# Kernel optimization log

Measured on AMD Instinct MI355X. Metric: run time of the kernel, lower is better.

## Reference

```python
import jax, jax.numpy as jnp
import numpy as np

B, S, D, H = 2, 2048, 2048, 16
HD = D // H
SCALE = 1.0 / np.sqrt(HD)


def setup_inputs() -> dict:
    key = jax.random.key(0)
    ks = jax.random.split(key, 11)
    xav = np.sqrt(6.0 / (D + D))  # xavier uniform bound for square weights
    def w(k):
        return jax.random.uniform(k, (D, D), jnp.float32, -xav, xav)
    return {
        "query": jax.random.normal(ks[0], (B, S, D), jnp.float32),
        "key": jax.random.normal(ks[1], (B, S, D), jnp.float32),
        "value": jax.random.normal(ks[2], (B, S, D), jnp.float32),
        "Wq": w(ks[3]), "bq": jnp.zeros((D,), jnp.float32),
        "Wk": w(ks[4]), "bk": jnp.zeros((D,), jnp.float32),
        "Wv": w(ks[5]), "bv": jnp.zeros((D,), jnp.float32),
        "Wo": w(ks[6]), "bo": jnp.zeros((D,), jnp.float32),
    }


def reference(query, key, value, Wq, bq, Wk, bk, Wv, bv, Wo, bo):
    # projections (torch Linear: x @ W.T + b)
    q = query @ Wq.T + bq
    k = key @ Wk.T + bk
    v = value @ Wv.T + bv
    # [B, H, S, HD]
    q = q.reshape(B, S, H, HD).transpose(0, 2, 1, 3)
    k = k.reshape(B, S, H, HD).transpose(0, 2, 1, 3)
    v = v.reshape(B, S, H, HD).transpose(0, 2, 1, 3)
    scores = jnp.einsum("bhqd,bhkd->bhqk", q, k) * SCALE
    causal = jnp.triu(jnp.ones((S, S), bool), k=1)
    scores = jnp.where(causal, -jnp.inf, scores)
    attn = jax.nn.softmax(scores, axis=-1)  # dropout p=0.0 -> identity
    out = jnp.einsum("bhqk,bhkd->bhqd", attn, v)
    out = out.transpose(0, 2, 1, 3).reshape(B, S, D)
    return out @ Wo.T + bo
```

## Files before the change

### kernel.cpp

```cpp
#include <hip/hip_runtime.h>
#include <hip/hip_bf16.h>


#define LOG2E 1.44269504088896340736f

typedef __attribute__((ext_vector_type(8))) short short8;
typedef __attribute__((ext_vector_type(4))) short short4b;
typedef __attribute__((ext_vector_type(4))) float floatx4;

__device__ __forceinline__ short f2bf(float f) {
  unsigned int u = __builtin_bit_cast(unsigned int, f);
  u += 0x7FFFu + ((u >> 16) & 1u);
  return (short)(u >> 16);
}

__device__ __forceinline__ short4b pack4bf(float a, float b, float c, float d) {
  __hip_bfloat162 lo = __float22bfloat162_rn(float2{a, b});
  __hip_bfloat162 hi = __float22bfloat162_rn(float2{c, d});
  short4b r;
  r[0] = __builtin_bit_cast(short, lo.x); r[1] = __builtin_bit_cast(short, lo.y);
  r[2] = __builtin_bit_cast(short, hi.x); r[3] = __builtin_bit_cast(short, hi.y);
  return r;
}

__device__ __forceinline__ void gl_lds16(const void* g, void* l) {
  __builtin_amdgcn_global_load_lds(
      (const __attribute__((address_space(1))) unsigned int*)g,
      (__attribute__((address_space(3))) unsigned int*)l, 16, 0, 0);
}

__global__ __launch_bounds__(256) void cvt_k(
    const float* __restrict__ s0, const float* __restrict__ s1,
    const float* __restrict__ s2, const float* __restrict__ s3,
    unsigned short* __restrict__ d0, unsigned short* __restrict__ d1,
    unsigned short* __restrict__ d2, unsigned short* __restrict__ d3, int n)
{
  const float* s; unsigned short* d;
  switch (blockIdx.y) {
    case 0: s = s0; d = d0; break;
    case 1: s = s1; d = d1; break;
    case 2: s = s2; d = d2; break;
    default: s = s3; d = d3; break;
  }
  const int i = (blockIdx.x * 256 + threadIdx.x) * 8;
  if (i >= n) return;
  float4 a = *(const float4*)(s + i);
  float4 b = *(const float4*)(s + i + 4);
  short8 v = (short8){f2bf(a.x), f2bf(a.y), f2bf(a.z), f2bf(a.w),
                      f2bf(b.x), f2bf(b.y), f2bf(b.z), f2bf(b.w)};
  *(short8*)(d + i) = v;
}

template<bool OUT_BF16, bool VT_OUT>
__global__ __launch_bounds__(512, 1) void gemm8_k(
    const unsigned short* __restrict__ A, const unsigned short* __restrict__ Bt,
    const float* __restrict__ bias, void* __restrict__ Cptr,
    int M, int N, int K, float alpha)
{
  __shared__ __align__(16) unsigned short As[3][256 * 64];
  __shared__ __align__(16) unsigned short Bs[3][128 * 64];
  (void)M;

  const int tid  = threadIdx.x;
  const int lane = tid & 63;
  const int wave = tid >> 6;
  const int quad = lane >> 4;
  const int l16  = lane & 15;
  const int lx7  = l16 & 7;
  const int wm   = wave >> 1, wn = wave & 1;
  const long bm  = (long)blockIdx.y * 256;
  const long bn  = (long)blockIdx.x * 128;

  const unsigned short* gA[4]; int lAo[4];
  const unsigned short* gB[2]; int lBo[2];
#pragma unroll
  for (int j = 0; j < 4; ++j) {
    const int pa = ((j >> 1) * 16 + wave * 2 + (j & 1)) * 64 + lane;
    const int r = pa >> 3, cp = pa & 7, cs = cp ^ (r & 7);
    gA[j]  = A + (bm + r) * (long)K + cs * 8;
    lAo[j] = pa * 8;
  }
#pragma unroll
  for (int j = 0; j < 2; ++j) {
    const int pb = (wave * 2 + j) * 64 + lane;
    const int r = pb >> 3, cp = pb & 7, cs = cp ^ (r & 7);
    gB[j]  = Bt + (bn + r) * (long)K + cs * 8;
    lBo[j] = pb * 8;
  }

  floatx4 acc[4][4];
#pragma unroll
  for (int i = 0; i < 4; ++i)
#pragma unroll
    for (int j = 0; j < 4; ++j) acc[i][j] = (floatx4){0.f, 0.f, 0.f, 0.f};

  const int NT = K >> 6;

#pragma unroll
  for (int j = 0; j < 4; ++j) gl_lds16(gA[j], &As[0][lAo[j]]);
#pragma unroll
  for (int j = 0; j < 2; ++j) gl_lds16(gB[j], &Bs[0][lBo[j]]);
  if (NT > 1) {
#pragma unroll
    for (int j = 0; j < 4; ++j) gl_lds16(gA[j] + 64, &As[1][lAo[j]]);
#pragma unroll
    for (int j = 0; j < 2; ++j) gl_lds16(gB[j] + 64, &Bs[1][lBo[j]]);
    asm volatile("s_waitcnt vmcnt(6)" ::: "memory");
  } else {
    asm volatile("s_waitcnt vmcnt(0)" ::: "memory");
  }
  __builtin_amdgcn_s_barrier();

  int cur = 0;
  for (int t = 0; t < NT; ++t) {
    int nx2 = cur + 2; if (nx2 >= 3) nx2 -= 3;
    const long kk2 = (long)(t + 2) * 64;
    const bool st  = (t + 2) < NT;
    const unsigned short* Ab = As[cur];
    const unsigned short* Bb = Bs[cur];

    short8 af[4][2];
#pragma unroll
    for (int mt = 0; mt < 4; ++mt)
#pragma unroll
      for (int ks = 0; ks < 2; ++ks)
        af[mt][ks] = *(const short8*)&Ab[(wm * 64 + mt * 16 + l16) * 64 +
                                         (((ks * 4 + quad) ^ lx7) * 8)];
    short8 bf0, bf1;

    bf0 = *(const short8*)&Bb[(wn * 64 + l16) * 64 + (((quad) ^ lx7) * 8)];
    bf1 = *(const short8*)&Bb[(wn * 64 + l16) * 64 + (((4 + quad) ^ lx7) * 8)];
    if (st) { gl_lds16(gA[0] + kk2, &As[nx2][lAo[0]]);
              gl_lds16(gA[1] + kk2, &As[nx2][lAo[1]]); }
    __builtin_amdgcn_s_barrier();
    asm volatile("s_waitcnt lgkmcnt(0)");
    __builtin_amdgcn_s_setprio(1);
#pragma unroll
    for (int mt = 0; mt < 4; ++mt) {
      acc[mt][0] = __builtin_amdgcn_mfma_f32_16x16x32_bf16(af[mt][0], bf0, acc[mt][0], 0, 0, 0);
      acc[mt][0] = __builtin_amdgcn_mfma_f32_16x16x32_bf16(af[mt][1], bf1, acc[mt][0], 0, 0, 0);
    }
    __builtin_amdgcn_s_setprio(0);
    __builtin_amdgcn_s_barrier();

    bf0 = *(const short8*)&Bb[(wn * 64 + 16 + l16) * 64 + (((quad) ^ lx7) * 8)];
    bf1 = *(const short8*)&Bb[(wn * 64 + 16 + l16) * 64 + (((4 + quad) ^ lx7) * 8)];
    if (st) { gl_lds16(gA[2] + kk2, &As[nx2][lAo[2]]);
              gl_lds16(gA[3] + kk2, &As[nx2][lAo[3]]); }
    __builtin_amdgcn_s_barrier();
    asm volatile("s_waitcnt lgkmcnt(0)");
    __builtin_amdgcn_s_setprio(1);
#pragma unroll
    for (int mt = 0; mt < 4; ++mt) {
      acc[mt][1] = __builtin_amdgcn_mfma_f32_16x16x32_bf16(af[mt][0], bf0, acc[mt][1], 0, 0, 0);
      acc[mt][1] = __builtin_amdgcn_mfma_f32_16x16x32_bf16(af[mt][1], bf1, acc[mt][1], 0, 0, 0);
    }
    __builtin_amdgcn_s_setprio(0);
    __builtin_amdgcn_s_barrier();

    bf0 = *(const short8*)&Bb[(wn * 64 + 32 + l16) * 64 + (((quad) ^ lx7) * 8)];
    bf1 = *(const short8*)&Bb[(wn * 64 + 32 + l16) * 64 + (((4 + quad) ^ lx7) * 8)];
    if (st) { gl_lds16(gB[0] + kk2, &Bs[nx2][lBo[0]]);
              gl_lds16(gB[1] + kk2, &Bs[nx2][lBo[1]]); }
    __builtin_amdgcn_s_barrier();
    asm volatile("s_waitcnt lgkmcnt(0)");
    __builtin_amdgcn_s_setprio(1);
#pragma unroll
    for (int mt = 0; mt < 4; ++mt) {
      acc[mt][2] = __builtin_amdgcn_mfma_f32_16x16x32_bf16(af[mt][0], bf0, acc[mt][2], 0, 0, 0);
      acc[mt][2] = __builtin_amdgcn_mfma_f32_16x16x32_bf16(af[mt][1], bf1, acc[mt][2], 0, 0, 0);
    }
    __builtin_amdgcn_s_setprio(0);
    __builtin_amdgcn_s_barrier();

    bf0 = *(const short8*)&Bb[(wn * 64 + 48 + l16) * 64 + (((quad) ^ lx7) * 8)];
    bf1 = *(const short8*)&Bb[(wn * 64 + 48 + l16) * 64 + (((4 + quad) ^ lx7) * 8)];
    __builtin_amdgcn_s_barrier();
    asm volatile("s_waitcnt lgkmcnt(0)");
    __builtin_amdgcn_s_setprio(1);
#pragma unroll
    for (int mt = 0; mt < 4; ++mt) {
      acc[mt][3] = __builtin_amdgcn_mfma_f32_16x16x32_bf16(af[mt][0], bf0, acc[mt][3], 0, 0, 0);
      acc[mt][3] = __builtin_amdgcn_mfma_f32_16x16x32_bf16(af[mt][1], bf1, acc[mt][3], 0, 0, 0);
    }
    __builtin_amdgcn_s_setprio(0);
    if (t + 1 < NT) {
      if (st) asm volatile("s_waitcnt vmcnt(6)" ::: "memory");
      else    asm volatile("s_waitcnt vmcnt(0)" ::: "memory");
    }
    __builtin_amdgcn_s_barrier();

    cur = cur + 1 >= 3 ? 0 : cur + 1;
  }

  if (VT_OUT) {
    __syncthreads();
    unsigned short* Ct = &As[0][0];
#pragma unroll
    for (int nt = 0; nt < 4; ++nt) {
      const int col_l = wn * 64 + nt * 16 + l16;
      const float bval = bias[bn + col_l];
#pragma unroll
      for (int mt = 0; mt < 4; ++mt) {
        const int row_l = wm * 64 + mt * 16 + quad * 4;
#pragma unroll
        for (int rg = 0; rg < 4; ++rg)
          Ct[col_l * 264 + row_l + rg] = (unsigned short)f2bf((acc[mt][nt][rg] + bval) * alpha);
      }
    }
    __syncthreads();
    const int b  = (int)(bm >> 11);
    const int s0 = (int)(bm & 2047);
    const int d   = tid >> 2;
    const int seg = tid & 3;
    unsigned short* dst = (unsigned short*)Cptr +
        ((long)(b * 16 + blockIdx.x) * 128 + d) * 2048 + s0 + seg * 64;
    const unsigned short* src = &Ct[d * 264 + seg * 64];
#pragma unroll
    for (int c = 0; c < 8; ++c)
      *(uint4*)(dst + c * 8) = *(const uint4*)(src + c * 8);
  } else {
#pragma unroll
    for (int nt = 0; nt < 4; ++nt) {
      const long col = bn + wn * 64 + nt * 16 + l16;
      const float bval = bias[col];
#pragma unroll
      for (int mt = 0; mt < 4; ++mt) {
#pragma unroll
        for (int rg = 0; rg < 4; ++rg) {
          const long row = bm + wm * 64 + mt * 16 + quad * 4 + rg;
          const float v = (acc[mt][nt][rg] + bval) * alpha;
          if (OUT_BF16) ((unsigned short*)Cptr)[row * (long)N + col] = (unsigned short)f2bf(v);
          else          ((float*)Cptr)[row * (long)N + col] = v;
        }
      }
    }
  }
}

template<bool A_BF16, bool OUT_BF16, bool VT_OUT>
__global__ __launch_bounds__(256, 2) void gemm_bias_k(
    const void* __restrict__ Aptr, const float* __restrict__ Bt,
    const float* __restrict__ bias, void* __restrict__ Cptr,
    int M, int N, int K, float alpha)
{
  __shared__ __align__(16) unsigned short smem[128 * 136];
  unsigned short* As = smem;
  unsigned short* Bs = smem + 128 * 40;

  const int tid  = threadIdx.x;
  const int lane = tid & 63;
  const int wave = tid >> 6;
  const int quad = lane >> 4;
  const int l16  = lane & 15;
  const int wr   = wave >> 1, wc = wave & 1;
  const long bm  = (long)blockIdx.y * 128;
  const long bn  = (long)blockIdx.x * 128;

  floatx4 acc[4][4];
#pragma unroll
  for (int i = 0; i < 4; ++i)
#pragma unroll
    for (int j = 0; j < 4; ++j) acc[i][j] = (floatx4){0.f, 0.f, 0.f, 0.f};

  const int srow = tid >> 2;
  const int cc   = tid & 3;

  for (int k0 = 0; k0 < K; k0 += 32) {
    __syncthreads();
#pragma unroll
    for (int r = 0; r < 2; ++r) {
      const int row = srow + r * 64;
      short8 av, bv;
      if (A_BF16) {
        av = *(const short8*)((const unsigned short*)Aptr + (bm + row) * (long)K + k0 + cc * 8);
      } else {
        const float* ap = (const float*)Aptr + (bm + row) * (long)K + k0 + cc * 8;
        float4 f0 = *(const float4*)ap;
        float4 f1 = *(const float4*)(ap + 4);
        av = (short8){f2bf(f0.x), f2bf(f0.y), f2bf(f0.z), f2bf(f0.w),
                      f2bf(f1.x), f2bf(f1.y), f2bf(f1.z), f2bf(f1.w)};
      }
      {
        const float* bp = Bt + (bn + row) * (long)K + k0 + cc * 8;
        float4 g0 = *(const float4*)bp;
        float4 g1 = *(const float4*)(bp + 4);
        bv = (short8){f2bf(g0.x), f2bf(g0.y), f2bf(g0.z), f2bf(g0.w),
                      f2bf(g1.x), f2bf(g1.y), f2bf(g1.z), f2bf(g1.w)};
      }
      *(short8*)&As[row * 40 + cc * 8] = av;
      *(short8*)&Bs[row * 40 + cc * 8] = bv;
    }
    __syncthreads();

    short8 af[4], bf[4];
#pragma unroll
    for (int t = 0; t < 4; ++t) {
      af[t] = *(const short8*)&As[(wr * 64 + t * 16 + l16) * 40 + quad * 8];
      bf[t] = *(const short8*)&Bs[(wc * 64 + t * 16 + l16) * 40 + quad * 8];
    }
#pragma unroll
    for (int mt = 0; mt < 4; ++mt)
#pragma unroll
      for (int nt = 0; nt < 4; ++nt)
        acc[mt][nt] = __builtin_amdgcn_mfma_f32_16x16x32_bf16(af[mt], bf[nt], acc[mt][nt], 0, 0, 0);
  }

  if (VT_OUT) {
    __syncthreads();
    unsigned short* Ct = smem;
#pragma unroll
    for (int nt = 0; nt < 4; ++nt) {
      const long col = bn + wc * 64 + nt * 16 + l16;
      const float bval = bias[col];
      const int col_l = wc * 64 + nt * 16 + l16;
#pragma unroll
      for (int mt = 0; mt < 4; ++mt) {
        const int row_l = wr * 64 + mt * 16 + quad * 4;
#pragma unroll
        for (int rg = 0; rg < 4; ++rg)
          Ct[col_l * 136 + row_l + rg] = (unsigned short)f2bf((acc[mt][nt][rg] + bval) * alpha);
      }
    }
    __syncthreads();
    const int b  = (int)(bm >> 11);
    const int s0 = (int)(bm & 2047);
    const int r    = tid >> 1;
    const int half = tid & 1;
    unsigned short* dst = (unsigned short*)Cptr +
        ((long)(b * 16 + blockIdx.x) * 128 + r) * 2048 + s0 + half * 64;
    const unsigned short* src = &Ct[r * 136 + half * 64];
#pragma unroll
    for (int c = 0; c < 8; ++c)
      *(uint4*)(dst + c * 8) = *(const uint4*)(src + c * 8);
  } else {
#pragma unroll
    for (int nt = 0; nt < 4; ++nt) {
      const long col = bn + wc * 64 + nt * 16 + l16;
      const float bval = bias[col];
#pragma unroll
      for (int mt = 0; mt < 4; ++mt) {
#pragma unroll
        for (int rg = 0; rg < 4; ++rg) {
          const long row = bm + wr * 64 + mt * 16 + quad * 4 + rg;
          const float v = (acc[mt][nt][rg] + bval) * alpha;
          if (OUT_BF16) ((unsigned short*)Cptr)[row * (long)N + col] = (unsigned short)f2bf(v);
          else          ((float*)Cptr)[row * (long)N + col] = v;
        }
      }
    }
  }
}

__global__ __launch_bounds__(256, 2) void flash_attn_k(
    const unsigned short* __restrict__ Q,
    const unsigned short* __restrict__ Kp,
    const unsigned short* __restrict__ Vt,
    unsigned short* __restrict__ O)
{
  constexpr int S = 2048, D = 2048, HD = 128;
  constexpr int PS = 72;

  __shared__ __align__(16) unsigned short Ks[64 * 128];
  __shared__ __align__(16) unsigned short Vst[128 * 64];
  __shared__ __align__(16) unsigned short Ps[64 * PS];

  const int tid  = threadIdx.x;
  const int lane = tid & 63;
  const int w    = tid >> 6;
  const int quad = lane >> 4;
  const int l16  = lane & 15;
  const int lx7  = l16 & 7;

  const int bx  = blockIdx.x;
  const int by  = blockIdx.y;
  const int idx = by * 2 + (bx >> 3);
  const int bh  = (bx & 7) * 4 + (idx >> 4);
  const int qsel = idx & 15;

  const long headoff = (long)(bh >> 4) * S * D + (long)(bh & 15) * HD;
  const long vtoff   = (long)bh * HD * S;

  const unsigned short* gK[4]; unsigned short* lK[4];
  const unsigned short* gV[4]; unsigned short* lV[4];
#pragma unroll
  for (int i = 0; i < 4; ++i) {
    const int p = (w * 4 + i) * 64 + lane;
    { const int r = p >> 4, cp = p & 15, c = cp ^ (r & 7);
      gK[i] = Kp + headoff + (long)r * D + c * 8;  lK[i] = &Ks[p * 8]; }
    { const int r = p >> 3, cp = p & 7, c = cp ^ (r & 7);
      gV[i] = Vt + vtoff + (long)r * S + c * 8;    lV[i] = &Vst[p * 8]; }
  }

#pragma unroll 1
  for (int half = 0; half < 2; ++half) {
    const int qt = half ? (31 - qsel) : qsel;
    const int qbase = qt * 64;
    const int qrow  = qbase + w * 16 + l16;
    const int qloc  = w * 16 + l16;

    short8 aq[4];
    {
      const unsigned short* qp = Q + headoff + (long)qrow * D;
#pragma unroll
      for (int ks = 0; ks < 4; ++ks)
        aq[ks] = *(const short8*)(qp + ks * 32 + quad * 8);
    }

    floatx4 o_acc[8];
#pragma unroll
    for (int t = 0; t < 8; ++t) o_acc[t] = (floatx4){0.f, 0.f, 0.f, 0.f};
    float m_i = -INFINITY, l_i = 0.f;

    for (int kt = 0; kt <= qt; ++kt) {
      const int kbase = kt * 64;
      __syncthreads();
#pragma unroll
      for (int i = 0; i < 4; ++i) gl_lds16(gK[i] + (long)kbase * D, lK[i]);
#pragma unroll
      for (int i = 0; i < 4; ++i) gl_lds16(gV[i] + kbase, lV[i]);
      __syncthreads();

      floatx4 sc[4];
#pragma unroll
      for (int nt = 0; nt < 4; ++nt) sc[nt] = (floatx4){0.f, 0.f, 0.f, 0.f};
#pragma unroll
      for (int nt = 0; nt < 4; ++nt) {
        const int krow = nt * 16 + l16;
#pragma unroll
        for (int ks = 0; ks < 4; ++ks) {
          const int cp = (ks * 4 + quad) ^ lx7;
          short8 kf = *(const short8*)&Ks[krow * 128 + cp * 8];
          sc[nt] = __builtin_amdgcn_mfma_f32_16x16x32_bf16(kf, aq[ks], sc[nt], 0, 0, 0);
        }
      }

      float sv[4][4];
      float rmax = -INFINITY;
      if (kt == qt) {
        const int kg0 = kbase + quad * 4;
#pragma unroll
        for (int nt = 0; nt < 4; ++nt)
#pragma unroll
          for (int rg = 0; rg < 4; ++rg) {
            float v = sc[nt][rg];
            if (kg0 + nt * 16 + rg > qrow) v = -INFINITY;
            sv[nt][rg] = v;
            rmax = fmaxf(rmax, v);
          }
      } else {
#pragma unroll
        for (int nt = 0; nt < 4; ++nt)
#pragma unroll
          for (int rg = 0; rg < 4; ++rg) {
            sv[nt][rg] = sc[nt][rg];
            rmax = fmaxf(rmax, sc[nt][rg]);
          }
      }
      rmax = fmaxf(rmax, __shfl_xor(rmax, 16));
      rmax = fmaxf(rmax, __shfl_xor(rmax, 32));

      const float mn = fmaxf(m_i, rmax);
      const float al = exp2f(m_i - mn);
      m_i = mn;

      float rsum = 0.f;
#pragma unroll
      for (int nt = 0; nt < 4; ++nt) {
        float p0 = exp2f(sv[nt][0] - mn), p1 = exp2f(sv[nt][1] - mn);
        float p2 = exp2f(sv[nt][2] - mn), p3 = exp2f(sv[nt][3] - mn);
        rsum += (p0 + p1) + (p2 + p3);
        *(short4b*)&Ps[qloc * PS + nt * 16 + quad * 4] = pack4bf(p0, p1, p2, p3);
      }
      rsum += __shfl_xor(rsum, 16);
      rsum += __shfl_xor(rsum, 32);
      l_i = l_i * al + rsum;

      if (__any(al != 1.0f)) {
#pragma unroll
        for (int t = 0; t < 8; ++t)
#pragma unroll
          for (int rg = 0; rg < 4; ++rg) o_acc[t][rg] *= al;
      }

      short8 pf[2];
#pragma unroll
      for (int ks = 0; ks < 2; ++ks)
        pf[ks] = *(const short8*)&Ps[qloc * PS + ks * 32 + quad * 8];

#pragma unroll
      for (int t = 0; t < 8; ++t) {
        const int drow = t * 16 + l16;
#pragma unroll
        for (int ks = 0; ks < 2; ++ks) {
          const int cp = (ks * 4 + quad) ^ lx7;
          short8 vf = *(const short8*)&Vst[drow * 64 + cp * 8];
          o_acc[t] = __builtin_amdgcn_mfma_f32_16x16x32_bf16(vf, pf[ks], o_acc[t], 0, 0, 0);
        }
      }
    }

    const float rl = 1.0f / l_i;
    unsigned short* op = O + headoff + (long)qrow * D;
#pragma unroll
    for (int t = 0; t < 8; ++t) {
      *(short4b*)(op + t * 16 + quad * 4) =
          pack4bf(o_acc[t][0] * rl, o_acc[t][1] * rl, o_acc[t][2] * rl, o_acc[t][3] * rl);
    }
  }
}

extern "C" void kernel_launch(void* const* d_in, const int* in_sizes, int n_in,
                              void* d_out, int out_size, void* d_ws, size_t ws_size,
                              hipStream_t stream) {
  const float* query = (const float*)d_in[0];
  const float* key_  = (const float*)d_in[1];
  const float* value = (const float*)d_in[2];
  const float* Wq = (const float*)d_in[3];
  const float* bq = (const float*)d_in[4];
  const float* Wk = (const float*)d_in[5];
  const float* bk = (const float*)d_in[6];
  const float* Wv = (const float*)d_in[7];
  const float* bv = (const float*)d_in[8];
  const float* Wo = (const float*)d_in[9];
  const float* bo = (const float*)d_in[10];
  float* out = (float*)d_out;

  constexpr int Bz = 2, S = 2048, D = 2048;
  constexpr int M = Bz * S;
  constexpr long NELEM = (long)M * D;
  constexpr long WELEM = (long)D * D;

  const float qscale = 0.08838834764831845f * LOG2E;
  dim3 gridG(D / 128, M / 128);
  dim3 gridG8(D / 128, M / 256);

  const size_t need_full = (size_t)(6 * NELEM + 4 * WELEM) * 2;

  if (ws_size >= need_full) {
    unsigned short* Qp  = (unsigned short*)d_ws;
    unsigned short* Kp  = Qp + NELEM;
    unsigned short* Vt  = Kp + NELEM;
    unsigned short* Xq  = Vt + NELEM;
    unsigned short* Xk  = Xq + NELEM;
    unsigned short* Xv  = Xk + NELEM;
    unsigned short* Wqb = Xv + NELEM;
    unsigned short* Wkb = Wqb + WELEM;
    unsigned short* Wvb = Wkb + WELEM;
    unsigned short* Wob = Wvb + WELEM;
    unsigned short* Oa  = Xq;

    cvt_k<<<dim3(NELEM / (8 * 256), 3), 256, 0, stream>>>(
        query, key_, value, value, Xq, Xk, Xv, Xv, (int)NELEM);
    cvt_k<<<dim3(WELEM / (8 * 256), 4), 256, 0, stream>>>(
        Wq, Wk, Wv, Wo, Wqb, Wkb, Wvb, Wob, (int)WELEM);

    gemm8_k<true, false><<<gridG8, 512, 0, stream>>>(Xq, Wqb, bq, Qp, M, D, D, qscale);
    gemm8_k<true, false><<<gridG8, 512, 0, stream>>>(Xk, Wkb, bk, Kp, M, D, D, 1.0f);
    gemm8_k<true, true ><<<gridG8, 512, 0, stream>>>(Xv, Wvb, bv, Vt, M, D, D, 1.0f);

    flash_attn_k<<<dim3(16, 32), 256, 0, stream>>>(Qp, Kp, Vt, Oa);

    gemm8_k<false, false><<<gridG8, 512, 0, stream>>>(Oa, Wob, bo, out, M, D, D, 1.0f);
  } else {
    unsigned short* Qp = (unsigned short*)d_ws;
    unsigned short* Kp = Qp + NELEM;
    unsigned short* Vt = Kp + NELEM;
    unsigned short* Oa = Vt + NELEM;

    gemm_bias_k<false, true, false><<<gridG, 256, 0, stream>>>(query, Wq, bq, Qp, M, D, D, qscale);
    gemm_bias_k<false, true, false><<<gridG, 256, 0, stream>>>(key_,  Wk, bk, Kp, M, D, D, 1.0f);
    gemm_bias_k<false, true, true ><<<gridG, 256, 0, stream>>>(value, Wv, bv, Vt, M, D, D, 1.0f);

    flash_attn_k<<<dim3(16, 32), 256, 0, stream>>>(Qp, Kp, Vt, Oa);

    gemm_bias_k<true, false, false><<<gridG, 256, 0, stream>>>(Oa, Wo, bo, out, M, D, D, 1.0f);
  }
}
```

Baseline: 458.4 us.

## Double-buffer attention K/V, merge GEMM MFMA phases, swizzle GEMM blocks by XCD

The attention kernel now double-buffers the K and V tiles in LDS and prefetches the next tile while computing the current one, which removes a sync-load-sync stall per key tile. It also skips the rescale of the running max unless some row's max grows by more than 8 (in log2 units). The GEMM groups its four per-k-step MFMA phases into two, so there are fewer barriers and more B fragments are held in registers. It also remaps block indices so that blocks on the same XCD share A/B tiles in L2. The costs are higher LDS use, extra registers, and a looser max bound on the probabilities, which could affect bf16 precision.

```diff
diff --git a/kernel.cpp b/kernel.cpp
--- a/kernel.cpp
+++ b/kernel.cpp
@@ -68,8 +68,17 @@
   const int l16  = lane & 15;
   const int lx7  = l16 & 7;
   const int wm   = wave >> 1, wn = wave & 1;
-  const long bm  = (long)blockIdx.y * 256;
-  const long bn  = (long)blockIdx.x * 128;
+
+  int bx, by;
+  if (gridDim.x == 16 && gridDim.y == 16) {
+    const int lin  = (int)(blockIdx.y * 16 + blockIdx.x);
+    const int xcd  = lin & 7;
+    const int slot = lin >> 3;
+    bx = (xcd & 1) * 8 + (slot & 7);
+    by = (xcd >> 1) * 4 + (slot >> 3);
+  } else { bx = (int)blockIdx.x; by = (int)blockIdx.y; }
+  const long bm  = (long)by * 256;
+  const long bn  = (long)bx * 128;
 
   const unsigned short* gA[4]; int lAo[4];
   const unsigned short* gB[2]; int lBo[2];
@@ -126,62 +135,43 @@
       for (int ks = 0; ks < 2; ++ks)
         af[mt][ks] = *(const short8*)&Ab[(wm * 64 + mt * 16 + l16) * 64 +
                                          (((ks * 4 + quad) ^ lx7) * 8)];
-    short8 bf0, bf1;
-
-    bf0 = *(const short8*)&Bb[(wn * 64 + l16) * 64 + (((quad) ^ lx7) * 8)];
-    bf1 = *(const short8*)&Bb[(wn * 64 + l16) * 64 + (((4 + quad) ^ lx7) * 8)];
+
+    short8 bf00 = *(const short8*)&Bb[(wn * 64 +  0 + l16) * 64 + (((0 + quad) ^ lx7) * 8)];
+    short8 bf01 = *(const short8*)&Bb[(wn * 64 +  0 + l16) * 64 + (((4 + quad) ^ lx7) * 8)];
+    short8 bf10 = *(const short8*)&Bb[(wn * 64 + 16 + l16) * 64 + (((0 + quad) ^ lx7) * 8)];
+    short8 bf11 = *(const short8*)&Bb[(wn * 64 + 16 + l16) * 64 + (((4 + quad) ^ lx7) * 8)];
     if (st) { gl_lds16(gA[0] + kk2, &As[nx2][lAo[0]]);
-              gl_lds16(gA[1] + kk2, &As[nx2][lAo[1]]); }
+              gl_lds16(gA[1] + kk2, &As[nx2][lAo[1]]);
+              gl_lds16(gA[2] + kk2, &As[nx2][lAo[2]]); }
     __builtin_amdgcn_s_barrier();
     asm volatile("s_waitcnt lgkmcnt(0)");
     __builtin_amdgcn_s_setprio(1);
 #pragma unroll
     for (int mt = 0; mt < 4; ++mt) {
-      acc[mt][0] = __builtin_amdgcn_mfma_f32_16x16x32_bf16(af[mt][0], bf0, acc[mt][0], 0, 0, 0);
-      acc[mt][0] = __builtin_amdgcn_mfma_f32_16x16x32_bf16(af[mt][1], bf1, acc[mt][0], 0, 0, 0);
+      acc[mt][0] = __builtin_amdgcn_mfma_f32_16x16x32_bf16(af[mt][0], bf00, acc[mt][0], 0, 0, 0);
+      acc[mt][0] = __builtin_amdgcn_mfma_f32_16x16x32_bf16(af[mt][1], bf01, acc[mt][0], 0, 0, 0);
+      acc[mt][1] = __builtin_amdgcn_mfma_f32_16x16x32_bf16(af[mt][0], bf10, acc[mt][1], 0, 0, 0);
+      acc[mt][1] = __builtin_amdgcn_mfma_f32_16x16x32_bf16(af[mt][1], bf11, acc[mt][1], 0, 0, 0);
     }
     __builtin_amdgcn_s_setprio(0);
     __builtin_amdgcn_s_barrier();
 
-    bf0 = *(const short8*)&Bb[(wn * 64 + 16 + l16) * 64 + (((quad) ^ lx7) * 8)];
-    bf1 = *(const short8*)&Bb[(wn * 64 + 16 + l16) * 64 + (((4 + quad) ^ lx7) * 8)];
-    if (st) { gl_lds16(gA[2] + kk2, &As[nx2][lAo[2]]);
-              gl_lds16(gA[3] + kk2, &As[nx2][lAo[3]]); }
-    __builtin_amdgcn_s_barrier();
-    asm volatile("s_waitcnt lgkmcnt(0)");
-    __builtin_amdgcn_s_setprio(1);
-#pragma unroll
-    for (int mt = 0; mt < 4; ++mt) {
-      acc[mt][1] = __builtin_amdgcn_mfma_f32_16x16x32_bf16(af[mt][0], bf0, acc[mt][1], 0, 0, 0);
-      acc[mt][1] = __builtin_amdgcn_mfma_f32_16x16x32_bf16(af[mt][1], bf1, acc[mt][1], 0, 0, 0);
-    }
-    __builtin_amdgcn_s_setprio(0);
-    __builtin_amdgcn_s_barrier();
-
-    bf0 = *(const short8*)&Bb[(wn * 64 + 32 + l16) * 64 + (((quad) ^ lx7) * 8)];
-    bf1 = *(const short8*)&Bb[(wn * 64 + 32 + l16) * 64 + (((4 + quad) ^ lx7) * 8)];
-    if (st) { gl_lds16(gB[0] + kk2, &Bs[nx2][lBo[0]]);
+    bf00 = *(const short8*)&Bb[(wn * 64 + 32 + l16) * 64 + (((0 + quad) ^ lx7) * 8)];
+    bf01 = *(const short8*)&Bb[(wn * 64 + 32 + l16) * 64 + (((4 + quad) ^ lx7) * 8)];
+    bf10 = *(const short8*)&Bb[(wn * 64 + 48 + l16) * 64 + (((0 + quad) ^ lx7) * 8)];
+    bf11 = *(const short8*)&Bb[(wn * 64 + 48 + l16) * 64 + (((4 + quad) ^ lx7) * 8)];
+    if (st) { gl_lds16(gA[3] + kk2, &As[nx2][lAo[3]]);
+              gl_lds16(gB[0] + kk2, &Bs[nx2][lBo[0]]);
               gl_lds16(gB[1] + kk2, &Bs[nx2][lBo[1]]); }
     __builtin_amdgcn_s_barrier();
     asm volatile("s_waitcnt lgkmcnt(0)");
     __builtin_amdgcn_s_setprio(1);
 #pragma unroll
     for (int mt = 0; mt < 4; ++mt) {
-      acc[mt][2] = __builtin_amdgcn_mfma_f32_16x16x32_bf16(af[mt][0], bf0, acc[mt][2], 0, 0, 0);
-      acc[mt][2] = __builtin_amdgcn_mfma_f32_16x16x32_bf16(af[mt][1], bf1, acc[mt][2], 0, 0, 0);
-    }
-    __builtin_amdgcn_s_setprio(0);
-    __builtin_amdgcn_s_barrier();
-
-    bf0 = *(const short8*)&Bb[(wn * 64 + 48 + l16) * 64 + (((quad) ^ lx7) * 8)];
-    bf1 = *(const short8*)&Bb[(wn * 64 + 48 + l16) * 64 + (((4 + quad) ^ lx7) * 8)];
-    __builtin_amdgcn_s_barrier();
-    asm volatile("s_waitcnt lgkmcnt(0)");
-    __builtin_amdgcn_s_setprio(1);
-#pragma unroll
-    for (int mt = 0; mt < 4; ++mt) {
-      acc[mt][3] = __builtin_amdgcn_mfma_f32_16x16x32_bf16(af[mt][0], bf0, acc[mt][3], 0, 0, 0);
-      acc[mt][3] = __builtin_amdgcn_mfma_f32_16x16x32_bf16(af[mt][1], bf1, acc[mt][3], 0, 0, 0);
+      acc[mt][2] = __builtin_amdgcn_mfma_f32_16x16x32_bf16(af[mt][0], bf00, acc[mt][2], 0, 0, 0);
+      acc[mt][2] = __builtin_amdgcn_mfma_f32_16x16x32_bf16(af[mt][1], bf01, acc[mt][2], 0, 0, 0);
+      acc[mt][3] = __builtin_amdgcn_mfma_f32_16x16x32_bf16(af[mt][0], bf10, acc[mt][3], 0, 0, 0);
+      acc[mt][3] = __builtin_amdgcn_mfma_f32_16x16x32_bf16(af[mt][1], bf11, acc[mt][3], 0, 0, 0);
     }
     __builtin_amdgcn_s_setprio(0);
     if (t + 1 < NT) {
@@ -214,7 +204,7 @@
     const int d   = tid >> 2;
     const int seg = tid & 3;
     unsigned short* dst = (unsigned short*)Cptr +
-        ((long)(b * 16 + blockIdx.x) * 128 + d) * 2048 + s0 + seg * 64;
+        ((long)(b * 16 + bx) * 128 + d) * 2048 + s0 + seg * 64;
     const unsigned short* src = &Ct[d * 264 + seg * 64];
 #pragma unroll
     for (int c = 0; c < 8; ++c)
@@ -361,8 +351,8 @@
   constexpr int S = 2048, D = 2048, HD = 128;
   constexpr int PS = 72;
 
-  __shared__ __align__(16) unsigned short Ks[64 * 128];
-  __shared__ __align__(16) unsigned short Vst[128 * 64];
+  __shared__ __align__(16) unsigned short Ks[2][64 * 128];
+  __shared__ __align__(16) unsigned short Vst[2][128 * 64];
   __shared__ __align__(16) unsigned short Ps[64 * PS];
 
   const int tid  = threadIdx.x;
@@ -381,15 +371,15 @@
   const long headoff = (long)(bh >> 4) * S * D + (long)(bh & 15) * HD;
   const long vtoff   = (long)bh * HD * S;
 
-  const unsigned short* gK[4]; unsigned short* lK[4];
-  const unsigned short* gV[4]; unsigned short* lV[4];
+  const unsigned short* gK[4]; int oK[4];
+  const unsigned short* gV[4]; int oV[4];
 #pragma unroll
   for (int i = 0; i < 4; ++i) {
     const int p = (w * 4 + i) * 64 + lane;
     { const int r = p >> 4, cp = p & 15, c = cp ^ (r & 7);
-      gK[i] = Kp + headoff + (long)r * D + c * 8;  lK[i] = &Ks[p * 8]; }
+      gK[i] = Kp + headoff + (long)r * D + c * 8;  oK[i] = p * 8; }
     { const int r = p >> 3, cp = p & 7, c = cp ^ (r & 7);
-      gV[i] = Vt + vtoff + (long)r * S + c * 8;    lV[i] = &Vst[p * 8]; }
+      gV[i] = Vt + vtoff + (long)r * S + c * 8;    oV[i] = p * 8; }
   }
 
 #pragma unroll 1
@@ -412,28 +402,45 @@
     for (int t = 0; t < 8; ++t) o_acc[t] = (floatx4){0.f, 0.f, 0.f, 0.f};
     float m_i = -INFINITY, l_i = 0.f;
 
+#pragma unroll
+    for (int i = 0; i < 4; ++i) gl_lds16(gK[i], &Ks[0][oK[i]]);
+#pragma unroll
+    for (int i = 0; i < 4; ++i) gl_lds16(gV[i], &Vst[0][oV[i]]);
+
     for (int kt = 0; kt <= qt; ++kt) {
+      const int cur = kt & 1;
       const int kbase = kt * 64;
-      __syncthreads();
-#pragma unroll
-      for (int i = 0; i < 4; ++i) gl_lds16(gK[i] + (long)kbase * D, lK[i]);
-#pragma unroll
-      for (int i = 0; i < 4; ++i) gl_lds16(gV[i] + kbase, lV[i]);
-      __syncthreads();
+      if (kt < qt) {
+        const long kb = (long)(kt + 1) * 64;
+        const int nb = cur ^ 1;
+#pragma unroll
+        for (int i = 0; i < 4; ++i) gl_lds16(gK[i] + kb * D, &Ks[nb][oK[i]]);
+#pragma unroll
+        for (int i = 0; i < 4; ++i) gl_lds16(gV[i] + kb, &Vst[nb][oV[i]]);
+        asm volatile("s_waitcnt vmcnt(8)" ::: "memory");
+      } else {
+        asm volatile("s_waitcnt vmcnt(0)" ::: "memory");
+      }
+      __builtin_amdgcn_s_barrier();
+
+      const unsigned short* Kb = &Ks[cur][0];
+      const unsigned short* Vb = &Vst[cur][0];
 
       floatx4 sc[4];
 #pragma unroll
       for (int nt = 0; nt < 4; ++nt) sc[nt] = (floatx4){0.f, 0.f, 0.f, 0.f};
+      __builtin_amdgcn_s_setprio(1);
 #pragma unroll
       for (int nt = 0; nt < 4; ++nt) {
         const int krow = nt * 16 + l16;
 #pragma unroll
         for (int ks = 0; ks < 4; ++ks) {
           const int cp = (ks * 4 + quad) ^ lx7;
-          short8 kf = *(const short8*)&Ks[krow * 128 + cp * 8];
+          short8 kf = *(const short8*)&Kb[krow * 128 + cp * 8];
           sc[nt] = __builtin_amdgcn_mfma_f32_16x16x32_bf16(kf, aq[ks], sc[nt], 0, 0, 0);
         }
       }
+      __builtin_amdgcn_s_setprio(0);
 
       float sv[4][4];
       float rmax = -INFINITY;
@@ -460,15 +467,22 @@
       rmax = fmaxf(rmax, __shfl_xor(rmax, 16));
       rmax = fmaxf(rmax, __shfl_xor(rmax, 32));
 
-      const float mn = fmaxf(m_i, rmax);
-      const float al = exp2f(m_i - mn);
-      m_i = mn;
+      float al = 1.0f;
+      if (__any(rmax > m_i + 8.0f)) {
+        const float mn = fmaxf(m_i, rmax);
+        al = exp2f(m_i - mn);
+        m_i = mn;
+#pragma unroll
+        for (int t = 0; t < 8; ++t)
+#pragma unroll
+          for (int rg = 0; rg < 4; ++rg) o_acc[t][rg] *= al;
+      }
 
       float rsum = 0.f;
 #pragma unroll
       for (int nt = 0; nt < 4; ++nt) {
-        float p0 = exp2f(sv[nt][0] - mn), p1 = exp2f(sv[nt][1] - mn);
-        float p2 = exp2f(sv[nt][2] - mn), p3 = exp2f(sv[nt][3] - mn);
+        float p0 = exp2f(sv[nt][0] - m_i), p1 = exp2f(sv[nt][1] - m_i);
+        float p2 = exp2f(sv[nt][2] - m_i), p3 = exp2f(sv[nt][3] - m_i);
         rsum += (p0 + p1) + (p2 + p3);
         *(short4b*)&Ps[qloc * PS + nt * 16 + quad * 4] = pack4bf(p0, p1, p2, p3);
       }
@@ -476,28 +490,24 @@
       rsum += __shfl_xor(rsum, 32);
       l_i = l_i * al + rsum;
 
-      if (__any(al != 1.0f)) {
-#pragma unroll
-        for (int t = 0; t < 8; ++t)
-#pragma unroll
-          for (int rg = 0; rg < 4; ++rg) o_acc[t][rg] *= al;
-      }
-
       short8 pf[2];
 #pragma unroll
       for (int ks = 0; ks < 2; ++ks)
         pf[ks] = *(const short8*)&Ps[qloc * PS + ks * 32 + quad * 8];
 
+      __builtin_amdgcn_s_setprio(1);
 #pragma unroll
       for (int t = 0; t < 8; ++t) {
         const int drow = t * 16 + l16;
 #pragma unroll
         for (int ks = 0; ks < 2; ++ks) {
           const int cp = (ks * 4 + quad) ^ lx7;
-          short8 vf = *(const short8*)&Vst[drow * 64 + cp * 8];
+          short8 vf = *(const short8*)&Vb[drow * 64 + cp * 8];
           o_acc[t] = __builtin_amdgcn_mfma_f32_16x16x32_bf16(vf, pf[ks], o_acc[t], 0, 0, 0);
         }
       }
+      __builtin_amdgcn_s_setprio(0);
+      __builtin_amdgcn_s_barrier();
     }
 
     const float rl = 1.0f / l_i;
```

After: 424.8 us. -7.3%, faster.
